# Optimization experiments

Hardware: AMD Instinct MI355X
Metric: run time of the kernel (lower is better)

## Reference

```python
import jax, jax.numpy as jnp
import numpy as np

N_NODES = 50000


def sage_conv(h, src, dst, W_l, b_l, W_r):
    # PyG SAGEConv(mean): out = lin_l(mean_j x_j) + lin_r(x_i)
    msg = h[src]                                           # [E, d]
    agg = jax.ops.segment_sum(msg, dst, num_segments=N_NODES)
    cnt = jax.ops.segment_sum(jnp.ones((src.shape[0], 1), h.dtype), dst,
                              num_segments=N_NODES)
    agg = agg / jnp.maximum(cnt, 1.0)
    return agg @ W_l + b_l + h @ W_r


def setup_inputs() -> dict:
    key = jax.random.key(0)
    ks = jax.random.split(key, 12)
    node_dim, hid, feat_dim = 128, 128, 32
    E, EB = 800000, 200000
    s = lambda k, *sh: jax.random.normal(k, sh, jnp.float32) * 0.05
    return {
        "x": jax.random.normal(ks[0], (N_NODES, node_dim), jnp.float32),
        "edge_index": jax.random.randint(ks[1], (2, E), 0, N_NODES),
        "batch_edge_index": jax.random.randint(ks[2], (2, EB), 0, N_NODES),
        "feat_batch": jax.random.normal(ks[3], (EB, feat_dim), jnp.float32),
        "W1_l": s(ks[4], node_dim, hid), "b1": jnp.zeros((hid,), jnp.float32),
        "W1_r": s(ks[5], node_dim, hid),
        "W2_l": s(ks[6], hid, hid), "b2": jnp.zeros((hid,), jnp.float32),
        "W2_r": s(ks[7], hid, hid),
        "Wc1": s(ks[8], hid * 2 + feat_dim, hid),
        "bc1": jnp.zeros((hid,), jnp.float32),
        "Wc2": s(ks[9], hid, 1), "bc2": jnp.zeros((1,), jnp.float32),
    }


def reference(x, edge_index, batch_edge_index, feat_batch,
              W1_l, b1, W1_r, W2_l, b2, W2_r, Wc1, bc1, Wc2, bc2):
    src, dst = edge_index[0], edge_index[1]
    # encoder (dropout is identity at inference)
    h = jax.nn.relu(sage_conv(x, src, dst, W1_l, b1, W1_r))
    h = jax.nn.relu(sage_conv(h, src, dst, W2_l, b2, W2_r))
    # classifier over batch edges
    bs, bd = batch_edge_index[0], batch_edge_index[1]
    z = jnp.concatenate([h[bs], h[bd], feat_batch], axis=-1)  # [EB, 2*hid+feat]
    z = jax.nn.relu(z @ Wc1 + bc1)
    return (z @ Wc2 + bc2).reshape(-1)
```

## Files before the change

### kernel.cpp

```cpp
#include <hip/hip_runtime.h>

#define N_NODES 50000
#define SLOTS 64
#define NODES_PER_G 6250

typedef unsigned short ushort_t;
typedef unsigned int uint_t;
typedef ushort_t ushort8 __attribute__((ext_vector_type(8)));
typedef __bf16 bf16x8 __attribute__((ext_vector_type(8)));
typedef float f32x4 __attribute__((ext_vector_type(4)));

__device__ inline ushort_t f2bf(float f) {
  union { float f; uint_t u; } v; v.f = f;
  uint_t u = v.u;
  uint_t r = (u + 0x7fffu + ((u >> 16) & 1u)) >> 16;
  return (ushort_t)r;
}
__device__ inline uint_t pack2bf(float a, float b) {
  return (uint_t)f2bf(a) | ((uint_t)f2bf(b) << 16);
}
__device__ inline float bfup(ushort_t u) {
  union { uint_t u; float f; } v; v.u = (uint_t)u << 16; return v.f;
}


__global__ void k_fillconv(const int* __restrict__ src, const int* __restrict__ dst,
                           int* __restrict__ cursor, int* __restrict__ nbrf, int E,
                           const float* __restrict__ x, ushort_t* __restrict__ xb,
                           const float* __restrict__ feat, ushort_t* __restrict__ featb,
                           const float* __restrict__ W1l, const float* __restrict__ W1r,
                           ushort_t* __restrict__ wt1,
                           const float* __restrict__ W2l, const float* __restrict__ W2r,
                           ushort_t* __restrict__ wt2,
                           const float* __restrict__ Wc1, ushort_t* __restrict__ wtc) {
  const int bid = blockIdx.x, tid = threadIdx.x;
  if (bid < 3128) {
    const int g = bid & 7;
    const int c = bid >> 3;
    const int lo = g * NODES_PER_G, hi = lo + NODES_PER_G;
    #pragma unroll
    for (int p = 0; p < 8; ++p) {
      int e = c * 2048 + p * 256 + tid;
      if (e < E) {
        int d = dst[e];
        if (d >= lo && d < hi) {
          int pos = atomicAdd(&cursor[d], 1);
          if (pos < SLOTS) nbrf[d * SLOTS + pos] = src[e];
        }
      }
    }
  } else if (bid < 3128 + 6250) {
    int t = (bid - 3128) * 256 + tid;
    float4 v = *(const float4*)(x + (size_t)t * 4);
    uint2 p; p.x = pack2bf(v.x, v.y); p.y = pack2bf(v.z, v.w);
    *(uint2*)(xb + (size_t)t * 4) = p;
  } else if (bid < 3128 + 12500) {
    int t = (bid - 3128 - 6250) * 256 + tid;
    float4 v = *(const float4*)(feat + (size_t)t * 4);
    uint2 p; p.x = pack2bf(v.x, v.y); p.y = pack2bf(v.z, v.w);
    *(uint2*)(featb + (size_t)t * 4) = p;
  } else {
    int t = (bid - 3128 - 12500) * 256 + tid;
    if (t < 32768) {
      int c = t >> 8, k = t & 255;
      wt1[t] = f2bf(k < 128 ? W1l[k * 128 + c] : W1r[(k - 128) * 128 + c]);
    } else if (t < 65536) {
      int t2 = t - 32768; int c = t2 >> 8, k = t2 & 255;
      wt2[t2] = f2bf(k < 128 ? W2l[k * 128 + c] : W2r[(k - 128) * 128 + c]);
    } else if (t < 65536 + 36864) {
      int t3 = t - 65536; int c = t3 / 288, k = t3 % 288;
      wtc[t3] = f2bf(Wc1[k * 128 + c]);
    }
  }
}


__global__ __launch_bounds__(256)
void k_agg(const ushort_t* __restrict__ xb, const int* __restrict__ cnt,
           const int* __restrict__ nbrf, ushort_t* __restrict__ aggb, int n) {
  const int lane = threadIdx.x & 63;
  const int g = lane >> 4;
  const int l16 = lane & 15;
  const int w = (int)((blockIdx.x * blockDim.x + threadIdx.x) >> 6);
  const int nw = (int)((gridDim.x * blockDim.x) >> 6);
  for (int nd = 2 * w; nd < n; nd += 2 * nw) {
    const int d0 = min(cnt[nd], SLOTS);
    const int d1 = min(cnt[nd + 1], SLOTS);
    const int b0 = nd * SLOTS;
    const int b1 = (nd + 1) * SLOTS;
    float A0[8], A1[8];
    #pragma unroll
    for (int i = 0; i < 8; ++i) { A0[i] = 0.f; A1[i] = 0.f; }
    int j0 = 0, j1 = 0;
    while (j0 + 8 <= d0 && j1 + 8 <= d1) {
      int s00 = nbrf[b0 + j0 + g],     s01 = nbrf[b0 + j0 + 4 + g];
      int s10 = nbrf[b1 + j1 + g],     s11 = nbrf[b1 + j1 + 4 + g];
      ushort8 v00 = *(const ushort8*)(xb + (size_t)s00 * 128 + l16 * 8);
      ushort8 v01 = *(const ushort8*)(xb + (size_t)s01 * 128 + l16 * 8);
      ushort8 v10 = *(const ushort8*)(xb + (size_t)s10 * 128 + l16 * 8);
      ushort8 v11 = *(const ushort8*)(xb + (size_t)s11 * 128 + l16 * 8);
      #pragma unroll
      for (int i = 0; i < 8; ++i) {
        A0[i] += bfup(v00[i]); A0[i] += bfup(v01[i]);
        A1[i] += bfup(v10[i]); A1[i] += bfup(v11[i]);
      }
      j0 += 8; j1 += 8;
    }
    for (; j0 + 8 <= d0; j0 += 8) {
      int s0 = nbrf[b0 + j0 + g], s1 = nbrf[b0 + j0 + 4 + g];
      ushort8 v0 = *(const ushort8*)(xb + (size_t)s0 * 128 + l16 * 8);
      ushort8 v1 = *(const ushort8*)(xb + (size_t)s1 * 128 + l16 * 8);
      #pragma unroll
      for (int i = 0; i < 8; ++i) { A0[i] += bfup(v0[i]); A0[i] += bfup(v1[i]); }
    }
    if (j0 + 4 <= d0) {
      int s0 = nbrf[b0 + j0 + g];
      ushort8 v0 = *(const ushort8*)(xb + (size_t)s0 * 128 + l16 * 8);
      #pragma unroll
      for (int i = 0; i < 8; ++i) A0[i] += bfup(v0[i]);
      j0 += 4;
    }
    if (j0 < d0) {
      int rem = d0 - j0;
      int s0 = nbrf[b0 + j0 + min(g, rem - 1)];
      ushort8 v0 = *(const ushort8*)(xb + (size_t)s0 * 128 + l16 * 8);
      float m = (g < rem) ? 1.f : 0.f;
      #pragma unroll
      for (int i = 0; i < 8; ++i) A0[i] += m * bfup(v0[i]);
    }
    for (; j1 + 8 <= d1; j1 += 8) {
      int s0 = nbrf[b1 + j1 + g], s1 = nbrf[b1 + j1 + 4 + g];
      ushort8 v0 = *(const ushort8*)(xb + (size_t)s0 * 128 + l16 * 8);
      ushort8 v1 = *(const ushort8*)(xb + (size_t)s1 * 128 + l16 * 8);
      #pragma unroll
      for (int i = 0; i < 8; ++i) { A1[i] += bfup(v0[i]); A1[i] += bfup(v1[i]); }
    }
    if (j1 + 4 <= d1) {
      int s0 = nbrf[b1 + j1 + g];
      ushort8 v0 = *(const ushort8*)(xb + (size_t)s0 * 128 + l16 * 8);
      #pragma unroll
      for (int i = 0; i < 8; ++i) A1[i] += bfup(v0[i]);
      j1 += 4;
    }
    if (j1 < d1) {
      int rem = d1 - j1;
      int s0 = nbrf[b1 + j1 + min(g, rem - 1)];
      ushort8 v0 = *(const ushort8*)(xb + (size_t)s0 * 128 + l16 * 8);
      float m = (g < rem) ? 1.f : 0.f;
      #pragma unroll
      for (int i = 0; i < 8; ++i) A1[i] += m * bfup(v0[i]);
    }
    float inv0 = 1.0f / (float)max(d0, 1);
    float inv1 = 1.0f / (float)max(d1, 1);
    ushort8 o0, o1;
    #pragma unroll
    for (int i = 0; i < 8; ++i) {
      float t0 = A0[i], t1 = A1[i];
      t0 += __shfl_xor(t0, 16); t1 += __shfl_xor(t1, 16);
      t0 += __shfl_xor(t0, 32); t1 += __shfl_xor(t1, 32);
      o0[i] = f2bf(t0 * inv0);  o1[i] = f2bf(t1 * inv1);
    }
    if (g == 0) {
      *(ushort8*)(aggb + (size_t)nd * 128 + l16 * 8) = o0;
      *(ushort8*)(aggb + (size_t)(nd + 1) * 128 + l16 * 8) = o1;
    }
  }
}


__global__ __launch_bounds__(256)
void k_linear_mfma(const ushort_t* __restrict__ aggb, const ushort_t* __restrict__ xinb,
                   const ushort_t* __restrict__ wt, const float* __restrict__ bias,
                   ushort_t* __restrict__ houtb, int M) {
  __shared__ ushort_t rows[64][258];
  const int tid = threadIdx.x;
  const int lane = tid & 63;
  const int w = tid >> 6;
  const int l4 = lane & 15, lg = lane >> 4;

  bf16x8 bfrag[8][2];
  #pragma unroll
  for (int kt = 0; kt < 8; ++kt)
    #pragma unroll
    for (int ct = 0; ct < 2; ++ct) {
      int col = w * 32 + ct * 16 + l4;
      bfrag[kt][ct] = __builtin_bit_cast(bf16x8,
          *(const ushort8*)(wt + (size_t)col * 256 + kt * 32 + lg * 8));
    }
  const int col0 = w * 32 + l4, col1 = col0 + 16;
  const float b0 = bias[col0], b1 = bias[col1];

  const int niter = (M + 63) >> 6;
  for (int it = blockIdx.x; it < niter; it += gridDim.x) {
    const int m0 = it << 6;
    __syncthreads();
    #pragma unroll
    for (int c = 0; c < 8; ++c) {
      int q = c * 256 + tid;
      int e = q >> 5, ch = q & 31;
      int rg = min(m0 + e, M - 1);
      const ushort_t* p = (ch < 16) ? (aggb + (size_t)rg * 128 + ch * 8)
                                    : (xinb + (size_t)rg * 128 + (ch - 16) * 8);
      *(ushort8*)(&rows[e][ch * 8]) = *(const ushort8*)p;
    }
    __syncthreads();

    f32x4 acc[4][2];
    #pragma unroll
    for (int ms = 0; ms < 4; ++ms) { acc[ms][0] = (f32x4)0.f; acc[ms][1] = (f32x4)0.f; }
    #pragma unroll
    for (int kt = 0; kt < 8; ++kt) {
      bf16x8 af[4];
      #pragma unroll
      for (int ms = 0; ms < 4; ++ms)
        af[ms] = __builtin_bit_cast(bf16x8,
            *(const ushort8*)(&rows[ms * 16 + l4][kt * 32 + lg * 8]));
      #pragma unroll
      for (int ms = 0; ms < 4; ++ms) {
        acc[ms][0] = __builtin_amdgcn_mfma_f32_16x16x32_bf16(af[ms], bfrag[kt][0], acc[ms][0], 0, 0, 0);
        acc[ms][1] = __builtin_amdgcn_mfma_f32_16x16x32_bf16(af[ms], bfrag[kt][1], acc[ms][1], 0, 0, 0);
      }
    }
    #pragma unroll
    for (int ms = 0; ms < 4; ++ms)
      #pragma unroll
      for (int r = 0; r < 4; ++r) {
        int rg = m0 + ms * 16 + lg * 4 + r;
        if (rg < M) {
          houtb[(size_t)rg * 128 + col0] = f2bf(fmaxf(acc[ms][0][r] + b0, 0.f));
          houtb[(size_t)rg * 128 + col1] = f2bf(fmaxf(acc[ms][1][r] + b1, 0.f));
        }
      }
  }
}


__device__ __forceinline__ void cls_load(int m0, int tid, const int* __restrict__ bs,
                                         const int* __restrict__ bd,
                                         const ushort_t* __restrict__ h2b,
                                         const ushort_t* __restrict__ featb,
                                         int M, ushort8* r) {
  #pragma unroll
  for (int c = 0; c < 9; ++c) {
    int q = c * 256 + tid;
    if (q < 1024) {
      int e = q >> 4, ch = q & 15;
      int idx = bs[min(m0 + e, M - 1)];
      r[c] = *(const ushort8*)(h2b + (size_t)idx * 128 + ch * 8);
    } else if (q < 2048) {
      int q2 = q - 1024; int e = q2 >> 4, ch = q2 & 15;
      int idx = bd[min(m0 + e, M - 1)];
      r[c] = *(const ushort8*)(h2b + (size_t)idx * 128 + ch * 8);
    } else {
      int q2 = q - 2048; int e = q2 >> 2, ch = q2 & 3;
      int eg = min(m0 + e, M - 1);
      r[c] = *(const ushort8*)(featb + (size_t)eg * 32 + ch * 8);
    }
  }
}

__device__ __forceinline__ void cls_store(int tid, const ushort8* r, ushort_t (*rows)[296]) {
  #pragma unroll
  for (int c = 0; c < 9; ++c) {
    int q = c * 256 + tid;
    if (q < 1024) {
      int e = q >> 4, ch = q & 15;
      *(ushort8*)(&rows[e][ch * 8]) = r[c];
    } else if (q < 2048) {
      int q2 = q - 1024; int e = q2 >> 4, ch = q2 & 15;
      *(ushort8*)(&rows[e][128 + ch * 8]) = r[c];
    } else {
      int q2 = q - 2048; int e = q2 >> 2, ch = q2 & 3;
      *(ushort8*)(&rows[e][256 + ch * 8]) = r[c];
    }
  }
}

__global__ __launch_bounds__(256)
void k_cls_mfma(const ushort_t* __restrict__ h2b, const int* __restrict__ bs,
                const int* __restrict__ bd, const ushort_t* __restrict__ featb,
                const ushort_t* __restrict__ wt, const float* __restrict__ bc1,
                const float* __restrict__ Wc2, const float* __restrict__ bc2,
                float* __restrict__ out, int M) {
  __shared__ ushort_t rows[64][296];
  __shared__ float outs[64];
  const int tid = threadIdx.x;
  const int lane = tid & 63;
  const int w = tid >> 6;
  const int l4 = lane & 15, lg = lane >> 4;

  bf16x8 bfrag[9][2];
  #pragma unroll
  for (int kt = 0; kt < 9; ++kt)
    #pragma unroll
    for (int ct = 0; ct < 2; ++ct) {
      int col = w * 32 + ct * 16 + l4;
      bfrag[kt][ct] = __builtin_bit_cast(bf16x8,
          *(const ushort8*)(wt + (size_t)col * 288 + kt * 32 + lg * 8));
    }
  const int col0 = w * 32 + l4, col1 = col0 + 16;
  const float b0 = bc1[col0], b1 = bc1[col1];
  const float w20 = Wc2[col0], w21 = Wc2[col1];
  const float bc2v = bc2[0];

  const int niter = (M + 63) >> 6;
  const int gstep = gridDim.x;
  int it = blockIdx.x;
  ushort8 r[9];
  if (it < niter) cls_load(it << 6, tid, bs, bd, h2b, featb, M, r);

  while (it < niter) {
    const int m0 = it << 6;
    __syncthreads();
    cls_store(tid, r, rows);
    if (tid < 64) outs[tid] = 0.f;
    __syncthreads();
    const int itn = it + gstep;
    if (itn < niter) cls_load(itn << 6, tid, bs, bd, h2b, featb, M, r);

    f32x4 acc[4][2];
    #pragma unroll
    for (int ms = 0; ms < 4; ++ms) { acc[ms][0] = (f32x4)0.f; acc[ms][1] = (f32x4)0.f; }
    #pragma unroll
    for (int kt = 0; kt < 9; ++kt) {
      bf16x8 af[4];
      #pragma unroll
      for (int ms = 0; ms < 4; ++ms)
        af[ms] = __builtin_bit_cast(bf16x8,
            *(const ushort8*)(&rows[ms * 16 + l4][kt * 32 + lg * 8]));
      #pragma unroll
      for (int ms = 0; ms < 4; ++ms) {
        acc[ms][0] = __builtin_amdgcn_mfma_f32_16x16x32_bf16(af[ms], bfrag[kt][0], acc[ms][0], 0, 0, 0);
        acc[ms][1] = __builtin_amdgcn_mfma_f32_16x16x32_bf16(af[ms], bfrag[kt][1], acc[ms][1], 0, 0, 0);
      }
    }
    #pragma unroll
    for (int ms = 0; ms < 4; ++ms) {
      #pragma unroll
      for (int rr = 0; rr < 4; ++rr) {
        float z0 = fmaxf(acc[ms][0][rr] + b0, 0.f);
        float z1 = fmaxf(acc[ms][1][rr] + b1, 0.f);
        float v = z0 * w20 + z1 * w21;
        v += __shfl_xor(v, 1); v += __shfl_xor(v, 2);
        v += __shfl_xor(v, 4); v += __shfl_xor(v, 8);
        if (l4 == 0) atomicAdd(&outs[ms * 16 + lg * 4 + rr], v);
      }
    }
    __syncthreads();
    if (tid < 64 && m0 + tid < M) out[m0 + tid] = outs[tid] + bc2v;
    it = itn;
  }
}


extern "C" void kernel_launch(void* const* d_in, const int* in_sizes, int n_in,
                              void* d_out, int out_size, void* d_ws, size_t ws_size,
                              hipStream_t stream) {
  const float* x    = (const float*)d_in[0];
  const int*   ei   = (const int*)d_in[1];
  const int*   bei  = (const int*)d_in[2];
  const float* feat = (const float*)d_in[3];
  const float* W1l  = (const float*)d_in[4];
  const float* b1   = (const float*)d_in[5];
  const float* W1r  = (const float*)d_in[6];
  const float* W2l  = (const float*)d_in[7];
  const float* b2   = (const float*)d_in[8];
  const float* W2r  = (const float*)d_in[9];
  const float* Wc1  = (const float*)d_in[10];
  const float* bc1  = (const float*)d_in[11];
  const float* Wc2  = (const float*)d_in[12];
  const float* bc2  = (const float*)d_in[13];
  float* out = (float*)d_out;

  const int E  = in_sizes[1] / 2;
  const int EB = in_sizes[2] / 2;
  const int* src = ei;
  const int* dst = ei + E;
  const int* bs = bei;
  const int* bd = bei + EB;

  char* ws = (char*)d_ws;
  int*      cursor = (int*)(ws + 0);
  int*      nbrf   = (int*)(ws + (1ull  << 20));
  ushort_t* xb     = (ushort_t*)(ws + (16ull << 20));
  ushort_t* aggb   = (ushort_t*)(ws + (32ull << 20));
  ushort_t* h1b    = (ushort_t*)(ws + (48ull << 20));
  ushort_t* h2b    = (ushort_t*)(ws + (64ull << 20));
  ushort_t* featb  = (ushort_t*)(ws + (80ull << 20));
  ushort_t* wt1    = (ushort_t*)(ws + (96ull << 20));
  ushort_t* wt2    = (ushort_t*)(ws + (96ull << 20) + (128u << 10));
  ushort_t* wtc    = (ushort_t*)(ws + (96ull << 20) + (256u << 10));

  hipMemsetAsync(cursor, 0, N_NODES * sizeof(int), stream);

  k_fillconv<<<3128 + 12500 + 400, 256, 0, stream>>>(src, dst, cursor, nbrf, E,
                                                     x, xb, feat, featb,
                                                     W1l, W1r, wt1, W2l, W2r, wt2,
                                                     Wc1, wtc);

  k_agg<<<2048, 256, 0, stream>>>(xb, cursor, nbrf, aggb, N_NODES);
  k_linear_mfma<<<782, 256, 0, stream>>>(aggb, xb, wt1, b1, h1b, N_NODES);
  k_agg<<<2048, 256, 0, stream>>>(h1b, cursor, nbrf, aggb, N_NODES);
  k_linear_mfma<<<782, 256, 0, stream>>>(aggb, h1b, wt2, b2, h2b, N_NODES);
  k_cls_mfma<<<1024, 256, 0, stream>>>(h2b, bs, bd, featb, wtc, bc1, Wc2, bc2, out, EB);
}
```

Measured before the change: 188.4 us.

## Bucket classifier edges by source-node range and move feat conversion into agg

Classifier edges are partitioned into 8 buckets by source-node range, using a per-block counting scatter in the fill kernel. Each classifier block then handles one bucket, so its h2b gathers for the source side hit a narrower region and should get better cache locality. The feat-to-bf16 conversion moves out of the fill kernel into extra blocks of the first aggregation launch, to balance work across kernels. The cost is an extra indirection through perm and scattered output writes. A fixed per-bucket capacity of 32768 could silently drop edges if a bucket overflows; with uniform random indices each bucket holds about 25000 edges.

```diff
diff --git a/kernel.cpp b/kernel.cpp
--- a/kernel.cpp
+++ b/kernel.cpp
@@ -3,6 +3,7 @@
 #define N_NODES 50000
 #define SLOTS 64
 #define NODES_PER_G 6250
+#define CAP 32768
 
 typedef unsigned short ushort_t;
 typedef unsigned int uint_t;
@@ -27,12 +28,13 @@
 __global__ void k_fillconv(const int* __restrict__ src, const int* __restrict__ dst,
                            int* __restrict__ cursor, int* __restrict__ nbrf, int E,
                            const float* __restrict__ x, ushort_t* __restrict__ xb,
-                           const float* __restrict__ feat, ushort_t* __restrict__ featb,
                            const float* __restrict__ W1l, const float* __restrict__ W1r,
                            ushort_t* __restrict__ wt1,
                            const float* __restrict__ W2l, const float* __restrict__ W2r,
                            ushort_t* __restrict__ wt2,
-                           const float* __restrict__ Wc1, ushort_t* __restrict__ wtc) {
+                           const float* __restrict__ Wc1, ushort_t* __restrict__ wtc,
+                           const int* __restrict__ bs, int* __restrict__ bcur,
+                           int* __restrict__ perm, int EB) {
   const int bid = blockIdx.x, tid = threadIdx.x;
   if (bid < 3128) {
     const int g = bid & 7;
@@ -49,18 +51,13 @@
         }
       }
     }
-  } else if (bid < 3128 + 6250) {
+  } else if (bid < 9378) {
     int t = (bid - 3128) * 256 + tid;
     float4 v = *(const float4*)(x + (size_t)t * 4);
     uint2 p; p.x = pack2bf(v.x, v.y); p.y = pack2bf(v.z, v.w);
     *(uint2*)(xb + (size_t)t * 4) = p;
-  } else if (bid < 3128 + 12500) {
-    int t = (bid - 3128 - 6250) * 256 + tid;
-    float4 v = *(const float4*)(feat + (size_t)t * 4);
-    uint2 p; p.x = pack2bf(v.x, v.y); p.y = pack2bf(v.z, v.w);
-    *(uint2*)(featb + (size_t)t * 4) = p;
-  } else {
-    int t = (bid - 3128 - 12500) * 256 + tid;
+  } else if (bid < 9778) {
+    int t = (bid - 9378) * 256 + tid;
     if (t < 32768) {
       int c = t >> 8, k = t & 255;
       wt1[t] = f2bf(k < 128 ? W1l[k * 128 + c] : W1r[(k - 128) * 128 + c]);
@@ -71,18 +68,45 @@
       int t3 = t - 65536; int c = t3 / 288, k = t3 % 288;
       wtc[t3] = f2bf(Wc1[k * 128 + c]);
     }
+  } else {
+    __shared__ int lcnt[8];
+    __shared__ int lbase[8];
+    int t = (bid - 9778) * 256 + tid;
+    if (tid < 8) lcnt[tid] = 0;
+    __syncthreads();
+    int b = 0, pos = 0;
+    bool valid = (t < EB);
+    if (valid) {
+      b = bs[t] / NODES_PER_G;
+      pos = atomicAdd(&lcnt[b], 1);
+    }
+    __syncthreads();
+    if (tid < 8) lbase[tid] = lcnt[tid] ? atomicAdd(&bcur[tid], lcnt[tid]) : 0;
+    __syncthreads();
+    if (valid) {
+      int p = lbase[b] + pos;
+      if (p < CAP) perm[b * CAP + p] = t;
+    }
   }
 }
 
 
 __global__ __launch_bounds__(256)
 void k_agg(const ushort_t* __restrict__ xb, const int* __restrict__ cnt,
-           const int* __restrict__ nbrf, ushort_t* __restrict__ aggb, int n) {
+           const int* __restrict__ nbrf, ushort_t* __restrict__ aggb, int n,
+           const float* __restrict__ feat, ushort_t* __restrict__ featb, int aggblk) {
+  if ((int)blockIdx.x >= aggblk) {
+    int t = (blockIdx.x - aggblk) * 256 + threadIdx.x;
+    float4 v = *(const float4*)(feat + (size_t)t * 4);
+    uint2 p; p.x = pack2bf(v.x, v.y); p.y = pack2bf(v.z, v.w);
+    *(uint2*)(featb + (size_t)t * 4) = p;
+    return;
+  }
   const int lane = threadIdx.x & 63;
   const int g = lane >> 4;
   const int l16 = lane & 15;
-  const int w = (int)((blockIdx.x * blockDim.x + threadIdx.x) >> 6);
-  const int nw = (int)((gridDim.x * blockDim.x) >> 6);
+  const int w = (int)((blockIdx.x * 256 + threadIdx.x) >> 6);
+  const int nw = (int)((aggblk * 256) >> 6);
   for (int nd = 2 * w; nd < n; nd += 2 * nw) {
     const int d0 = min(cnt[nd], SLOTS);
     const int d1 = min(cnt[nd + 1], SLOTS);
@@ -235,26 +259,30 @@
 }
 
 
-__device__ __forceinline__ void cls_load(int m0, int tid, const int* __restrict__ bs,
+__device__ __forceinline__ void cls_load(int m0, int cnt, int tid,
+                                         const int* __restrict__ pb,
+                                         const int* __restrict__ bs,
                                          const int* __restrict__ bd,
                                          const ushort_t* __restrict__ h2b,
                                          const ushort_t* __restrict__ featb,
-                                         int M, ushort8* r) {
+                                         ushort8* r) {
   #pragma unroll
   for (int c = 0; c < 9; ++c) {
     int q = c * 256 + tid;
     if (q < 1024) {
       int e = q >> 4, ch = q & 15;
-      int idx = bs[min(m0 + e, M - 1)];
+      int orig = pb[min(m0 + e, cnt - 1)];
+      int idx = bs[orig];
       r[c] = *(const ushort8*)(h2b + (size_t)idx * 128 + ch * 8);
     } else if (q < 2048) {
       int q2 = q - 1024; int e = q2 >> 4, ch = q2 & 15;
-      int idx = bd[min(m0 + e, M - 1)];
+      int orig = pb[min(m0 + e, cnt - 1)];
+      int idx = bd[orig];
       r[c] = *(const ushort8*)(h2b + (size_t)idx * 128 + ch * 8);
     } else {
       int q2 = q - 2048; int e = q2 >> 2, ch = q2 & 3;
-      int eg = min(m0 + e, M - 1);
-      r[c] = *(const ushort8*)(featb + (size_t)eg * 32 + ch * 8);
+      int orig = pb[min(m0 + e, cnt - 1)];
+      r[c] = *(const ushort8*)(featb + (size_t)orig * 32 + ch * 8);
     }
   }
 }
@@ -279,9 +307,10 @@
 __global__ __launch_bounds__(256)
 void k_cls_mfma(const ushort_t* __restrict__ h2b, const int* __restrict__ bs,
                 const int* __restrict__ bd, const ushort_t* __restrict__ featb,
+                const int* __restrict__ perm, const int* __restrict__ ecnt,
                 const ushort_t* __restrict__ wt, const float* __restrict__ bc1,
                 const float* __restrict__ Wc2, const float* __restrict__ bc2,
-                float* __restrict__ out, int M) {
+                float* __restrict__ out) {
   __shared__ ushort_t rows[64][296];
   __shared__ float outs[64];
   const int tid = threadIdx.x;
@@ -303,11 +332,14 @@
   const float w20 = Wc2[col0], w21 = Wc2[col1];
   const float bc2v = bc2[0];
 
-  const int niter = (M + 63) >> 6;
-  const int gstep = gridDim.x;
-  int it = blockIdx.x;
+  const int bkt = blockIdx.x & 7;
+  const int* pb = perm + bkt * CAP;
+  const int cnt = min(ecnt[bkt], CAP);
+  const int niter = (cnt + 63) >> 6;
+  const int tstep = gridDim.x >> 3;
+  int it = blockIdx.x >> 3;
   ushort8 r[9];
-  if (it < niter) cls_load(it << 6, tid, bs, bd, h2b, featb, M, r);
+  if (it < niter) cls_load(it << 6, cnt, tid, pb, bs, bd, h2b, featb, r);
 
   while (it < niter) {
     const int m0 = it << 6;
@@ -315,8 +347,8 @@
     cls_store(tid, r, rows);
     if (tid < 64) outs[tid] = 0.f;
     __syncthreads();
-    const int itn = it + gstep;
-    if (itn < niter) cls_load(itn << 6, tid, bs, bd, h2b, featb, M, r);
+    const int itn = it + tstep;
+    if (itn < niter) cls_load(itn << 6, cnt, tid, pb, bs, bd, h2b, featb, r);
 
     f32x4 acc[4][2];
     #pragma unroll
@@ -347,7 +379,7 @@
       }
     }
     __syncthreads();
-    if (tid < 64 && m0 + tid < M) out[m0 + tid] = outs[tid] + bc2v;
+    if (tid < 64 && m0 + tid < cnt) out[pb[m0 + tid]] = outs[tid] + bc2v;
     it = itn;
   }
 }
@@ -381,7 +413,9 @@
 
   char* ws = (char*)d_ws;
   int*      cursor = (int*)(ws + 0);
-  int*      nbrf   = (int*)(ws + (1ull  << 20));
+  int*      bcur   = (int*)(ws + 200704);
+  int*      perm   = (int*)(ws + (256u << 10));
+  int*      nbrf   = (int*)(ws + (2ull  << 20));
   ushort_t* xb     = (ushort_t*)(ws + (16ull << 20));
   ushort_t* aggb   = (ushort_t*)(ws + (32ull << 20));
   ushort_t* h1b    = (ushort_t*)(ws + (48ull << 20));
@@ -391,16 +425,15 @@
   ushort_t* wt2    = (ushort_t*)(ws + (96ull << 20) + (128u << 10));
   ushort_t* wtc    = (ushort_t*)(ws + (96ull << 20) + (256u << 10));
 
-  hipMemsetAsync(cursor, 0, N_NODES * sizeof(int), stream);
-
-  k_fillconv<<<3128 + 12500 + 400, 256, 0, stream>>>(src, dst, cursor, nbrf, E,
-                                                     x, xb, feat, featb,
-                                                     W1l, W1r, wt1, W2l, W2r, wt2,
-                                                     Wc1, wtc);
-
-  k_agg<<<2048, 256, 0, stream>>>(xb, cursor, nbrf, aggb, N_NODES);
+  hipMemsetAsync(cursor, 0, 200736, stream);
+
+  k_fillconv<<<10560, 256, 0, stream>>>(src, dst, cursor, nbrf, E,
+                                        x, xb, W1l, W1r, wt1, W2l, W2r, wt2,
+                                        Wc1, wtc, bs, bcur, perm, EB);
+
+  k_agg<<<2048 + 6250, 256, 0, stream>>>(xb, cursor, nbrf, aggb, N_NODES, feat, featb, 2048);
   k_linear_mfma<<<782, 256, 0, stream>>>(aggb, xb, wt1, b1, h1b, N_NODES);
-  k_agg<<<2048, 256, 0, stream>>>(h1b, cursor, nbrf, aggb, N_NODES);
+  k_agg<<<2048, 256, 0, stream>>>(h1b, cursor, nbrf, aggb, N_NODES, nullptr, nullptr, 2048);
   k_linear_mfma<<<782, 256, 0, stream>>>(aggb, h1b, wt2, b2, h2b, N_NODES);
-  k_cls_mfma<<<1024, 256, 0, stream>>>(h2b, bs, bd, featb, wtc, bc1, Wc2, bc2, out, EB);
-}
+  k_cls_mfma<<<1024, 256, 0, stream>>>(h2b, bs, bd, featb, perm, bcur, wtc, bc1, Wc2, bc2, out);
+}
```

New measurement: 198.6 us. 1.05x slower.
